# Kernel optimization log

Hardware: AMD Instinct MI355X
Metric: run time of the kernel (lower is better)

The kernel has to match this reference:

```python
import jax, jax.numpy as jnp
import numpy as np

N, C, H, W = 4, 256, 100, 100
COUT, G, EPS = 256, 32, 1e-5
K = 9  # 3x3 kernel positions

# regular 3x3 grid: row0 = dy, row1 = dx (mmcv offset convention)
REG = jnp.array([[-1,-1,-1,0,0,0,1,1,1],
                 [-1, 0, 1,-1,0,1,-1,0,1]], dtype=jnp.float32)  # (2,9)
KY = jnp.array([0,0,0,1,1,1,2,2,2], dtype=jnp.float32)
KX = jnp.array([0,1,2,0,1,2,0,1,2], dtype=jnp.float32)


def conv3x3(x, w, b):
    out = jax.lax.conv_general_dilated(x, w, window_strides=(1,1),
                                       padding=((1,1),(1,1)),
                                       dimension_numbers=('NCHW','OIHW','NCHW'))
    return out + b[None, :, None, None]


def setup_inputs() -> dict:
    key = jax.random.key(0)
    ks = jax.random.split(key, 7)
    x = jax.random.normal(ks[0], (N, C, H, W), dtype=jnp.float32)
    w_tm = jax.random.normal(ks[1], (4, C, 3, 3), dtype=jnp.float32) * 0.01
    b_tm = jnp.zeros((4,), dtype=jnp.float32)
    w_tr = jax.random.normal(ks[2], (2, C, 3, 3), dtype=jnp.float32) * 0.01
    b_tr = jnp.zeros((2,), dtype=jnp.float32)
    w_def = jax.random.normal(ks[3], (COUT, C, 3, 3), dtype=jnp.float32) * (1.0 / np.sqrt(C * 9.0))
    gn_w = 1.0 + 0.1 * jax.random.normal(ks[4], (COUT,), dtype=jnp.float32)
    gn_b = 0.1 * jax.random.normal(ks[5], (COUT,), dtype=jnp.float32)
    return dict(x=x, w_tm=w_tm, b_tm=b_tm, w_tr=w_tr, b_tr=b_tr,
                w_def=w_def, gn_w=gn_w, gn_b=gn_b)


def _compute_offsets(x, w_tm, b_tm, w_tr, b_tr):
    tm = conv3x3(x, w_tm, b_tm)                      # (N,4,H,W)
    tr = conv3x3(x, w_tr, b_tr)                      # (N,2,H,W)
    A = tm.transpose(0, 2, 3, 1).reshape(N, H, W, 2, 2)
    off = jnp.einsum('nhwij,jk->nhwik', A, REG) - REG  # (N,H,W,2,9)
    dy = (off[:, :, :, 0, :] + tr[:, 0][..., None]).transpose(0, 3, 1, 2)  # (N,9,H,W)
    dx = (off[:, :, :, 1, :] + tr[:, 1][..., None]).transpose(0, 3, 1, 2)
    return dy, dx


def _bilinear_sample(img, ys, xs):
    # img: (C,H,W); ys/xs: (9,H,W) float sampling coords; zero pad outside.
    y0 = jnp.floor(ys); x0 = jnp.floor(xs)
    wy = ys - y0; wx = xs - x0
    y0i = y0.astype(jnp.int32); x0i = x0.astype(jnp.int32)
    def gather(yi, xi):
        valid = (yi >= 0) & (yi < H) & (xi >= 0) & (xi < W)
        yc = jnp.clip(yi, 0, H - 1); xc = jnp.clip(xi, 0, W - 1)
        return img[:, yc, xc] * valid[None].astype(img.dtype)  # (C,9,H,W)
    v00 = gather(y0i,     x0i)
    v01 = gather(y0i,     x0i + 1)
    v10 = gather(y0i + 1, x0i)
    v11 = gather(y0i + 1, x0i + 1)
    return (v00 * (1 - wy) * (1 - wx) + v01 * (1 - wy) * wx
            + v10 * wy * (1 - wx) + v11 * wy * wx)


def _forward(x, w_tm, b_tm, w_tr, b_tr, w_def, gn_w, gn_b):
    dy, dx = _compute_offsets(x, w_tm, b_tm, w_tr, b_tr)
    # sampling positions: p*stride - pad + k*dil + offset  (stride=1, pad=dil=1)
    ys = jnp.arange(H, dtype=jnp.float32)[None, :, None] - 1.0 + KY[:, None, None] + dy
    xs = jnp.arange(W, dtype=jnp.float32)[None, None, :] - 1.0 + KX[:, None, None] + dx
    sampled = jax.vmap(_bilinear_sample)(x, ys, xs)       # (N,C,9,H,W)
    out = jnp.einsum('nckhw,ock->nohw', sampled, w_def.reshape(COUT, C, K))
    # GroupNorm(32) + ReLU
    g = out.reshape(N, G, (COUT // G) * H * W)
    mu = g.mean(axis=2, keepdims=True)
    var = g.var(axis=2, keepdims=True)
    g = (g - mu) * jax.lax.rsqrt(var + EPS)
    out = g.reshape(N, COUT, H, W) * gn_w[None, :, None, None] + gn_b[None, :, None, None]
    return jax.nn.relu(out)


def reference(x, w_tm, b_tm, w_tr, b_tr, w_def, gn_w, gn_b):
    return _forward(x, w_tm, b_tm, w_tr, b_tr, w_def, gn_w, gn_b)
```

## Files before the change

### kernel.cpp

```cpp
#include <hip/hip_runtime.h>
#include <math.h>

#define C_IN  256
#define HH    100
#define WW    100
#define HW    10000
#define NBAT  4
#define COUTC 256
#define K9    9
#define GG    32
#define TYN   13
#define TXN   9
#define NT2   117
#define NWG   468
#define EPSF  1e-5f

typedef _Float16 f16x8 __attribute__((ext_vector_type(8)));
typedef _Float16 h2v   __attribute__((ext_vector_type(2)));
typedef float    f32x4 __attribute__((ext_vector_type(4)));

__global__ void __launch_bounds__(256) k0_weights(const float* __restrict__ wd,
                                                  const float* __restrict__ w_tm,
                                                  const float* __restrict__ w_tr,
                                                  _Float16* __restrict__ wf,
                                                  _Float16* __restrict__ wf6) {
  const int b = blockIdx.x;
  if (b < 2304) {
    const int i = b * 256 + threadIdx.x;
    const int j  = i & 7;
    const int l  = (i >> 3) & 63;
    const int ot = (i >> 9) & 15;
    const int q  = i >> 13;
    const int tap = q >> 3, cg = q & 7;
    const int o = ot * 16 + (l & 15);
    const int c = cg * 32 + (l >> 4) * 8 + j;
    wf[i] = (_Float16)wd[((size_t)o * C_IN + c) * K9 + tap];
  } else {
    const int i = (b - 2304) * 256 + threadIdx.x;
    const int j = i & 7, l = (i >> 3) & 63, q = i >> 9;
    const int tap = q >> 3, cg = q & 7;
    const int o = l & 15;
    const int c = cg * 32 + (l >> 4) * 8 + j;
    float v = 0.f;
    if (o < 4)      v = w_tm[((size_t)o * C_IN + c) * K9 + tap];
    else if (o < 6) v = w_tr[((size_t)(o - 4) * C_IN + c) * K9 + tap];
    wf6[i] = (_Float16)v;
  }
}

__global__ void __launch_bounds__(256) kt_nhwc(const float* __restrict__ x,
                                               _Float16* __restrict__ xh) {
  __shared__ float T[64][65];
  const int b = blockIdx.x;
  const int n = b / (4 * 157);
  const int r = b % (4 * 157);
  const int cg = r / 157, tile = r % 157;
  const int pbase = tile * 64, c0 = cg * 64;
  const int tid = threadIdx.x, lane = tid & 63, wv = tid >> 6;

#pragma unroll 4
  for (int i = 0; i < 16; ++i) {
    const int c = c0 + wv * 16 + i;
    const int pix = pbase + lane;
    T[wv * 16 + i][lane] = (pix < HW) ? x[((size_t)n * C_IN + c) * HW + pix] : 0.f;
  }
  __syncthreads();

  const int cl = tid & 15;
#pragma unroll
  for (int j = 0; j < 4; ++j) {
    const int pxl = (tid >> 4) + j * 16;
    const int pix = pbase + pxl;
    if (pix < HW) {
      const float v0 = T[cl * 4 + 0][pxl], v1 = T[cl * 4 + 1][pxl];
      const float v2 = T[cl * 4 + 2][pxl], v3 = T[cl * 4 + 3][pxl];
      uint2 pk;
      h2v a = {(_Float16)v0, (_Float16)v1};
      h2v bq = {(_Float16)v2, (_Float16)v3};
      pk.x = __builtin_bit_cast(unsigned, a);
      pk.y = __builtin_bit_cast(unsigned, bq);
      *(uint2*)(xh + ((size_t)n * HW + pix) * C_IN + c0 + cl * 4) = pk;
    }
  }
}

#define RAW_BARRIER()                                                         \
  asm volatile("s_waitcnt lgkmcnt(0)" ::: "memory");                          \
  __builtin_amdgcn_sched_barrier(0);                                          \
  __builtin_amdgcn_s_barrier();                                               \
  __builtin_amdgcn_sched_barrier(0);

__global__ void __launch_bounds__(256) k1_off(
    const _Float16* __restrict__ xh, const _Float16* __restrict__ wf6,
    const float* __restrict__ b_tm, const float* __restrict__ b_tr,
    float* __restrict__ posy, float* __restrict__ posx) {
  const int ob = blockIdx.x;
  const int xcd = ob & 7, loc = ob >> 3;
  const int sblk = (xcd < 1 ? xcd * 79 : 79 + (xcd - 1) * 78) + loc;
  const int tid = threadIdx.x, lane = tid & 63, wv = tid >> 6;
  const int s = sblk * 4 + wv;
  const int n = s / 625, strip = s % 625;
  const int ps = strip * 16;
  const int px = ps + (lane & 15);
  const int h = px / WW, w = px % WW;
  const char* xbase = (const char*)(xh + (size_t)n * HW * C_IN) + (lane >> 4) * 16;

  int nbA, nbB; bool vA, vB;
#define K1NB(T_, NB, V)                                                       \
  { const int y = h + (T_) / 3 - 1, xx = w + (T_) % 3 - 1;                    \
    V = ((unsigned)y < (unsigned)HH) && ((unsigned)xx < (unsigned)WW);        \
    NB = (V ? (y * WW + xx) : 0) * 512; }

  uint4 q0, q1, q2, q3;
  K1NB(0, nbA, vA)
  nbB = nbA; vB = vA;
  q0 = *(const uint4*)(xbase + nbA + 0 * 64);
  q1 = *(const uint4*)(xbase + nbA + 1 * 64);
  q2 = *(const uint4*)(xbase + nbA + 2 * 64);
  q3 = *(const uint4*)(xbase + nbA + 3 * 64);
  f16x8 afA = *(const f16x8*)(wf6 + (size_t)0 * 512 + lane * 8);
  f16x8 afB = *(const f16x8*)(wf6 + (size_t)1 * 512 + lane * 8);

  f32x4 acc = (f32x4)(0.f);
  const uint4 z4 = {0u, 0u, 0u, 0u};

#define K1SUB(CG, Q, AF)                                                      \
  {                                                                           \
    const int p = t * 8 + (CG);                                               \
    uint4 bq = vA ? Q : z4;                                                   \
    f16x8 bf = __builtin_bit_cast(f16x8, bq);                                 \
    if ((CG) == 2) { K1NB((t < 8 ? t + 1 : 8), nbB, vB) }                     \
    if ((CG) < 4) { Q = *(const uint4*)(xbase + nbA + ((CG) + 4) * 64); }     \
    else if (t < 8) { Q = *(const uint4*)(xbase + nbB + ((CG) - 4) * 64); }   \
    acc = __builtin_amdgcn_mfma_f32_16x16x32_f16(AF, bf, acc, 0, 0, 0);       \
    if ((CG) < 6 || t < 8)                                                    \
      AF = *(const f16x8*)(wf6 + (size_t)(p + 2) * 512 + lane * 8);           \
  }

  for (int t = 0; t < 9; ++t) {
    K1SUB(0, q0, afA) K1SUB(1, q1, afB) K1SUB(2, q2, afA) K1SUB(3, q3, afB)
    K1SUB(4, q0, afA) K1SUB(5, q1, afB) K1SUB(6, q2, afA) K1SUB(7, q3, afB)
    nbA = nbB; vA = vB;
  }

  const float t0v = __shfl(acc[0], (lane & 15) + 16);
  const float t1v = __shfl(acc[1], (lane & 15) + 16);
  if (lane < 16) {
    const float A00 = acc[0] + b_tm[0], A01 = acc[1] + b_tm[1];
    const float A10 = acc[2] + b_tm[2], A11 = acc[3] + b_tm[3];
    const float t0 = t0v + b_tr[0], t1 = t1v + b_tr[1];
    const float fh = (float)h, fw = (float)w;
#pragma unroll
    for (int k = 0; k < 9; ++k) {
      const float ry = (float)(k / 3 - 1);
      const float rx = (float)(k % 3 - 1);
      posy[((size_t)n * K9 + k) * HW + px] = fh + t0 + A00 * ry + A01 * rx;
      posx[((size_t)n * K9 + k) * HW + px] = fw + t1 + A10 * ry + A11 * rx;
    }
  }
}

__global__ void __launch_bounds__(512, 4) k2_deform(
    const _Float16* __restrict__ xh, const _Float16* __restrict__ wfrag,
    const float* __restrict__ posy, const float* __restrict__ posx,
    float* __restrict__ out, float* __restrict__ part) {
  __shared__ __align__(16) char Bs[2 * 96 * 64];
  __shared__ __align__(16) unsigned int ctab[864 * 8];

  const int ob = blockIdx.x;
  const int xcd = ob & 7, loc = ob >> 3;
  const int wg = (xcd < 4 ? xcd * 59 : 236 + (xcd - 4) * 58) + loc;
  const int n = wg / NT2, rem = wg % NT2;
  const int ty = rem / TXN, tx = rem % TXN;

  const int tid = threadIdx.x, lane = tid & 63, wv = tid >> 6;
  const bool stg = tid < 384;
  const int px_s = tid >> 2, qo = tid & 3;
  const int wsw = (((qo + (px_s >> 1)) & 3) << 4);
  const int rpx = lane & 15, rko = lane >> 4;
  const int rsw = (((rko + (rpx >> 1)) & 3) << 4);

  for (int s = tid; s < 864; s += 512) {
    const int tap = s / 96, j = s % 96;
    const int row = ty * 8 + j / 12, col = tx * 12 + j % 12;
    const bool pvv = (row < HH) && (col < WW);
    const int mpa = pvv ? (row * WW + col) : 0;
    float ys = posy[((size_t)n * K9 + tap) * HW + mpa];
    float xs = posx[((size_t)n * K9 + tap) * HW + mpa];
    if (!pvv) { ys = -1e4f; xs = -1e4f; }
    const float y0f = floorf(ys), x0f = floorf(xs);
    const float wy = ys - y0f, wx = xs - x0f;
    const int iy0 = (int)y0f, ix0 = (int)x0f;
    const bool vy0 = ((unsigned)iy0 < (unsigned)HH);
    const bool vy1 = ((unsigned)(iy0 + 1) < (unsigned)HH);
    const bool vx0 = ((unsigned)ix0 < (unsigned)WW);
    const bool vx1 = ((unsigned)(ix0 + 1) < (unsigned)WW);
    const bool v0 = vy0 && vx0, v1 = vy0 && vx1;
    const bool v2 = vy1 && vx0, v3 = vy1 && vx1;
    uint4 oa, wa;
    oa.x = (v0 ? (iy0 * WW + ix0) : 0) * 512u;
    oa.y = (v1 ? (iy0 * WW + ix0 + 1) : 0) * 512u;
    oa.z = (v2 ? ((iy0 + 1) * WW + ix0) : 0) * 512u;
    oa.w = (v3 ? ((iy0 + 1) * WW + ix0 + 1) : 0) * 512u;
    const float g0 = v0 ? (1.f - wy) * (1.f - wx) : 0.f;
    const float g1 = v1 ? (1.f - wy) * wx : 0.f;
    const float g2 = v2 ? wy * (1.f - wx) : 0.f;
    const float g3 = v3 ? wy * wx : 0.f;
    const _Float16 h0 = (_Float16)g0, h1 = (_Float16)g1;
    const _Float16 h2_ = (_Float16)g2, h3 = (_Float16)g3;
    wa.x = __builtin_bit_cast(unsigned, (h2v){h0, h0});
    wa.y = __builtin_bit_cast(unsigned, (h2v){h1, h1});
    wa.z = __builtin_bit_cast(unsigned, (h2v){h2_, h2_});
    wa.w = __builtin_bit_cast(unsigned, (h2v){h3, h3});
    uint4* cp = (uint4*)&ctab[s * 8];
    cp[0] = oa;
    cp[1] = wa;
  }
  __syncthreads();

  const char* xbase = (const char*)(xh + (size_t)n * HW * C_IN);

  uint4 O, Wt, c0, c1, c2, c3;
  f16x8 aA0, aA1, aB0, aB1;

#define ISSUE(S)                                                              \
  if (stg) {                                                                  \
    const uint4* ce = (const uint4*)&ctab[(((S) >> 3) * 96 + px_s) * 8];      \
    O = ce[0];                                                                \
    Wt = ce[1];                                                               \
    const int choff = ((S) & 7) * 64 + qo * 16;                               \
    c0 = *(const uint4*)(xbase + O.x + choff);                                \
    c1 = *(const uint4*)(xbase + O.y + choff);                                \
    c2 = *(const uint4*)(xbase + O.z + choff);                                \
    c3 = *(const uint4*)(xbase + O.w + choff);                                \
  }

#define CW1(c)                                                                \
  __builtin_bit_cast(unsigned,                                                \
      (h2v)(w0 * __builtin_bit_cast(h2v, c0.c) +                              \
            w1 * __builtin_bit_cast(h2v, c1.c) +                              \
            w2 * __builtin_bit_cast(h2v, c2.c) +                              \
            w3 * __builtin_bit_cast(h2v, c3.c)))

#define COMBINE_WRITE(BUFW)                                                   \
  if (stg) {                                                                  \
    h2v w0 = __builtin_bit_cast(h2v, Wt.x), w1 = __builtin_bit_cast(h2v, Wt.y); \
    h2v w2 = __builtin_bit_cast(h2v, Wt.z), w3 = __builtin_bit_cast(h2v, Wt.w); \
    uint4 sv;                                                                 \
    sv.x = CW1(x);                                                            \
    sv.y = CW1(y);                                                            \
    sv.z = CW1(z);                                                            \
    sv.w = CW1(w);                                                            \
    *(uint4*)(Bs + (BUFW) * 6144 + px_s * 64 + wsw) = sv;                     \
  }

#define LOADA(A0_, A1_, CK)                                                   \
  {                                                                           \
    const _Float16* wfp = wfrag + (((size_t)(CK) * 16 + wv * 2) * 64 + lane) * 8; \
    A0_ = *(const f16x8*)(wfp);                                               \
    A1_ = *(const f16x8*)(wfp + 512);                                         \
  }

  f32x4 acc[2][6];
#pragma unroll
  for (int ot = 0; ot < 2; ++ot)
#pragma unroll
    for (int bt = 0; bt < 6; ++bt) acc[ot][bt] = (f32x4)(0.f);

#define MF(a, bx, o_, b_) \
  acc[o_][b_] = __builtin_amdgcn_mfma_f32_16x16x32_f16(a, bx, acc[o_][b_], 0, 0, 0);

#define MFMA12(A0_, A1_, BUF)                                                 \
  {                                                                           \
    const char* bb = Bs + (BUF) * 6144 + rpx * 64 + rsw;                      \
    f16x8 b0 = *(const f16x8*)(bb);                                           \
    f16x8 b1 = *(const f16x8*)(bb + 1024);                                    \
    f16x8 b2 = *(const f16x8*)(bb + 2048);                                    \
    f16x8 b3 = *(const f16x8*)(bb + 3072);                                    \
    f16x8 b4 = *(const f16x8*)(bb + 4096);                                    \
    f16x8 b5 = *(const f16x8*)(bb + 5120);                                    \
    __builtin_amdgcn_s_setprio(1);                                            \
    MF(A0_, b0, 0, 0) MF(A1_, b0, 1, 0)                                       \
    MF(A0_, b1, 0, 1) MF(A1_, b1, 1, 1)                                       \
    MF(A0_, b2, 0, 2) MF(A1_, b2, 1, 2)                                       \
    MF(A0_, b3, 0, 3) MF(A1_, b3, 1, 3)                                       \
    MF(A0_, b4, 0, 4) MF(A1_, b4, 1, 4)                                       \
    MF(A0_, b5, 0, 5) MF(A1_, b5, 1, 5)                                       \
    __builtin_amdgcn_s_setprio(0);                                            \
  }

  ISSUE(0)
  COMBINE_WRITE(0)
  ISSUE(1)
  LOADA(aA0, aA1, 0)
  LOADA(aB0, aB1, 1)
  RAW_BARRIER()

  for (int sp = 0; sp < 35; ++sp) {
    const int s0 = 2 * sp, s1 = 2 * sp + 1;
    MFMA12(aA0, aA1, 0)
    LOADA(aA0, aA1, s0 + 2)
    COMBINE_WRITE(1)
    ISSUE(s0 + 2)
    RAW_BARRIER()
    MFMA12(aB0, aB1, 1)
    LOADA(aB0, aB1, s1 + 2)
    COMBINE_WRITE(0)
    ISSUE(s1 + 2)
    RAW_BARRIER()
  }
  MFMA12(aA0, aA1, 0)
  COMBINE_WRITE(1)
  RAW_BARRIER()
  MFMA12(aB0, aB1, 1)

  float* grA = (float*)ctab;
  float* grB = grA + 1024;
  const int colb = lane & 15, prow = (lane >> 4) * 4;
#pragma unroll
  for (int ot = 0; ot < 2; ++ot) {
    float s1 = 0.f, s2 = 0.f;
#pragma unroll
    for (int bt = 0; bt < 6; ++bt) {
      const int jj = bt * 16 + colb;
      const int row = ty * 8 + jj / 12, col = tx * 12 + jj % 12;
      const f32x4 a = acc[ot][bt];
      if (row < HH && col < WW) {
        float* op = out + ((size_t)(n * COUTC + wv * 32 + ot * 16 + prow)) * HW +
                    row * WW + col;
        op[0] = a[0];
        op[HW] = a[1];
        op[2 * HW] = a[2];
        op[3 * HW] = a[3];
      }
      s1 += a[0] + a[1] + a[2] + a[3];
      s2 += a[0] * a[0] + a[1] * a[1] + a[2] * a[2] + a[3] * a[3];
    }
    grA[(wv * 2 + ot) * 64 + lane] = s1;
    grB[(wv * 2 + ot) * 64 + lane] = s2;
  }
  __syncthreads();
  if (tid < 32) {
    const int wv2 = tid >> 2, ot2 = (tid >> 1) & 1, hb = tid & 1;
    float a1 = 0.f, a2 = 0.f;
#pragma unroll 8
    for (int l = 0; l < 32; ++l) {
      a1 += grA[(wv2 * 2 + ot2) * 64 + hb * 32 + l];
      a2 += grB[(wv2 * 2 + ot2) * 64 + hb * 32 + l];
    }
    float* pp = part + (((size_t)n * NT2 + rem) * GG + tid) * 2;
    pp[0] = a1;
    pp[1] = a2;
  }
}

__global__ void __launch_bounds__(64) k3_stats(const float* __restrict__ part,
                                               float* __restrict__ stats) {
  const int b = blockIdx.x;
  const int n = b >> 5, g = b & 31;
  double s = 0.0, q = 0.0;
  for (int i = threadIdx.x; i < NT2; i += 64) {
    const float* pp = part + (((size_t)n * NT2 + i) * GG + g) * 2;
    s += pp[0];
    q += pp[1];
  }
#pragma unroll
  for (int off = 32; off > 0; off >>= 1) {
    s += __shfl_down(s, off);
    q += __shfl_down(q, off);
  }
  if (threadIdx.x == 0) {
    const double cnt = 8.0 * (double)HW;
    const double mean = s / cnt;
    const double var = q / cnt - mean * mean;
    stats[b * 2 + 0] = (float)mean;
    stats[b * 2 + 1] = (float)(1.0 / sqrt(var + (double)EPSF));
  }
}

__global__ void __launch_bounds__(256) k4_norm(float* __restrict__ out,
                                               const float* __restrict__ stats,
                                               const float* __restrict__ gw,
                                               const float* __restrict__ gb) {
  const size_t i4 = (size_t)blockIdx.x * 256 + threadIdx.x;
  const size_t idx = i4 * 4;
  const int n = (int)(idx / ((size_t)COUTC * HW));
  const int r = (int)(idx % ((size_t)COUTC * HW));
  const int o = r / HW;
  const int g = o >> 3;
  const float mean = stats[(n * GG + g) * 2 + 0];
  const float rs = stats[(n * GG + g) * 2 + 1];
  const float sc = rs * gw[o];
  const float sh = gb[o] - mean * sc;
  float4 v = *(float4*)(out + idx);
  v.x = fmaxf(fmaf(v.x, sc, sh), 0.f);
  v.y = fmaxf(fmaf(v.y, sc, sh), 0.f);
  v.z = fmaxf(fmaf(v.z, sc, sh), 0.f);
  v.w = fmaxf(fmaf(v.w, sc, sh), 0.f);
  *(float4*)(out + idx) = v;
}

extern "C" void kernel_launch(void* const* d_in, const int* in_sizes, int n_in,
                              void* d_out, int out_size, void* d_ws, size_t ws_size,
                              hipStream_t stream) {
  const float* x    = (const float*)d_in[0];
  const float* w_tm = (const float*)d_in[1];
  const float* b_tm = (const float*)d_in[2];
  const float* w_tr = (const float*)d_in[3];
  const float* b_tr = (const float*)d_in[4];
  const float* w_def = (const float*)d_in[5];
  const float* gn_w = (const float*)d_in[6];
  const float* gn_b = (const float*)d_in[7];
  float* out = (float*)d_out;
  float* ws = (float*)d_ws;

  float* posy  = ws;
  float* posx  = ws + 360000;
  _Float16* wfrag = (_Float16*)(ws + 720000);
  _Float16* wf6   = (_Float16*)(ws + 1014912);
  _Float16* xh    = (_Float16*)(ws + 1033344);
  float* part  = ws + 6153344;
  float* stats = ws + 6183296;

  hipLaunchKernelGGL(k0_weights, dim3(2448), dim3(256), 0, stream,
                     w_def, w_tm, w_tr, wfrag, wf6);
  hipLaunchKernelGGL(kt_nhwc, dim3(2512), dim3(256), 0, stream, x, xh);
  hipLaunchKernelGGL(k1_off, dim3(625), dim3(256), 0, stream,
                     xh, wf6, b_tm, b_tr, posy, posx);
  hipLaunchKernelGGL(k2_deform, dim3(NWG), dim3(512), 0, stream,
                     xh, wfrag, posy, posx, out, part);
  hipLaunchKernelGGL(k3_stats, dim3(NBAT * GG), dim3(64), 0, stream, part, stats);
  hipLaunchKernelGGL(k4_norm, dim3(10000), dim3(256), 0, stream,
                     out, stats, gn_w, gn_b);
}
```

Baseline: 137.4 us.

## Merge prep kernels, fold stats into norm, deepen gather prefetch, nontemporal stores

Combines the weight repack and the NHWC transpose into one launch, and removes the separate GroupNorm stats kernel by having every norm block reduce the per-tile partials itself. In the deform kernel, the gather pipeline now runs one stage further ahead using two register sets, and the combine weights are read from LDS only when needed. Conv outputs are written with nontemporal stores. The aim is fewer launches and better hiding of gather latency, at the cost of redundant partial reductions in every norm block (float instead of double), more live registers, and a nontemporal hint on data that k4 reads back.

New measurement: 204.2 us. 1.49x slower.

```diff
diff --git a/kernel.cpp b/kernel.cpp
--- a/kernel.cpp
+++ b/kernel.cpp
@@ -19,39 +19,40 @@
 typedef _Float16 h2v   __attribute__((ext_vector_type(2)));
 typedef float    f32x4 __attribute__((ext_vector_type(4)));
 
-__global__ void __launch_bounds__(256) k0_weights(const float* __restrict__ wd,
-                                                  const float* __restrict__ w_tm,
-                                                  const float* __restrict__ w_tr,
-                                                  _Float16* __restrict__ wf,
-                                                  _Float16* __restrict__ wf6) {
+__global__ void __launch_bounds__(256) kt_prep(const float* __restrict__ x,
+                                               const float* __restrict__ wd,
+                                               const float* __restrict__ w_tm,
+                                               const float* __restrict__ w_tr,
+                                               _Float16* __restrict__ xh,
+                                               _Float16* __restrict__ wf,
+                                               _Float16* __restrict__ wf6) {
   const int b = blockIdx.x;
-  if (b < 2304) {
-    const int i = b * 256 + threadIdx.x;
-    const int j  = i & 7;
-    const int l  = (i >> 3) & 63;
-    const int ot = (i >> 9) & 15;
-    const int q  = i >> 13;
-    const int tap = q >> 3, cg = q & 7;
-    const int o = ot * 16 + (l & 15);
-    const int c = cg * 32 + (l >> 4) * 8 + j;
-    wf[i] = (_Float16)wd[((size_t)o * C_IN + c) * K9 + tap];
-  } else {
-    const int i = (b - 2304) * 256 + threadIdx.x;
-    const int j = i & 7, l = (i >> 3) & 63, q = i >> 9;
-    const int tap = q >> 3, cg = q & 7;
-    const int o = l & 15;
-    const int c = cg * 32 + (l >> 4) * 8 + j;
-    float v = 0.f;
-    if (o < 4)      v = w_tm[((size_t)o * C_IN + c) * K9 + tap];
-    else if (o < 6) v = w_tr[((size_t)(o - 4) * C_IN + c) * K9 + tap];
-    wf6[i] = (_Float16)v;
-  }
-}
-
-__global__ void __launch_bounds__(256) kt_nhwc(const float* __restrict__ x,
-                                               _Float16* __restrict__ xh) {
+  if (b >= 2512) {
+    const int bb = b - 2512;
+    if (bb < 2304) {
+      const int i = bb * 256 + threadIdx.x;
+      const int j  = i & 7;
+      const int l  = (i >> 3) & 63;
+      const int ot = (i >> 9) & 15;
+      const int q  = i >> 13;
+      const int tap = q >> 3, cg = q & 7;
+      const int o = ot * 16 + (l & 15);
+      const int c = cg * 32 + (l >> 4) * 8 + j;
+      wf[i] = (_Float16)wd[((size_t)o * C_IN + c) * K9 + tap];
+    } else {
+      const int i = (bb - 2304) * 256 + threadIdx.x;
+      const int j = i & 7, l = (i >> 3) & 63, q = i >> 9;
+      const int tap = q >> 3, cg = q & 7;
+      const int o = l & 15;
+      const int c = cg * 32 + (l >> 4) * 8 + j;
+      float v = 0.f;
+      if (o < 4)      v = w_tm[((size_t)o * C_IN + c) * K9 + tap];
+      else if (o < 6) v = w_tr[((size_t)(o - 4) * C_IN + c) * K9 + tap];
+      wf6[i] = (_Float16)v;
+    }
+    return;
+  }
   __shared__ float T[64][65];
-  const int b = blockIdx.x;
   const int n = b / (4 * 157);
   const int r = b % (4 * 157);
   const int cg = r / 157, tile = r % 157;
@@ -220,38 +221,39 @@
 
   const char* xbase = (const char*)(xh + (size_t)n * HW * C_IN);
 
-  uint4 O, Wt, c0, c1, c2, c3;
+  uint4 cA0, cA1, cA2, cA3, cB0, cB1, cB2, cB3;
   f16x8 aA0, aA1, aB0, aB1;
 
-#define ISSUE(S)                                                              \
+#define ISSUE(S, C0, C1, C2, C3)                                              \
   if (stg) {                                                                  \
-    const uint4* ce = (const uint4*)&ctab[(((S) >> 3) * 96 + px_s) * 8];      \
-    O = ce[0];                                                                \
-    Wt = ce[1];                                                               \
+    const uint4 Ox = *(const uint4*)&ctab[(((S) >> 3) * 96 + px_s) * 8];      \
     const int choff = ((S) & 7) * 64 + qo * 16;                               \
-    c0 = *(const uint4*)(xbase + O.x + choff);                                \
-    c1 = *(const uint4*)(xbase + O.y + choff);                                \
-    c2 = *(const uint4*)(xbase + O.z + choff);                                \
-    c3 = *(const uint4*)(xbase + O.w + choff);                                \
-  }
-
-#define CW1(c)                                                                \
+    C0 = *(const uint4*)(xbase + Ox.x + choff);                               \
+    C1 = *(const uint4*)(xbase + Ox.y + choff);                               \
+    C2 = *(const uint4*)(xbase + Ox.z + choff);                               \
+    C3 = *(const uint4*)(xbase + Ox.w + choff);                               \
+  }
+
+#define CW1(c, C0, C1, C2, C3)                                                \
   __builtin_bit_cast(unsigned,                                                \
-      (h2v)(w0 * __builtin_bit_cast(h2v, c0.c) +                              \
-            w1 * __builtin_bit_cast(h2v, c1.c) +                              \
-            w2 * __builtin_bit_cast(h2v, c2.c) +                              \
-            w3 * __builtin_bit_cast(h2v, c3.c)))
-
-#define COMBINE_WRITE(BUFW)                                                   \
+      (h2v)(w0 * __builtin_bit_cast(h2v, C0.c) +                              \
+            w1 * __builtin_bit_cast(h2v, C1.c) +                              \
+            w2 * __builtin_bit_cast(h2v, C2.c) +                              \
+            w3 * __builtin_bit_cast(h2v, C3.c)))
+
+#define COMBINE_WRITE(S, C0, C1, C2, C3)                                      \
   if (stg) {                                                                  \
-    h2v w0 = __builtin_bit_cast(h2v, Wt.x), w1 = __builtin_bit_cast(h2v, Wt.y); \
-    h2v w2 = __builtin_bit_cast(h2v, Wt.z), w3 = __builtin_bit_cast(h2v, Wt.w); \
+    const uint4 Wt = *(const uint4*)&ctab[(((S) >> 3) * 96 + px_s) * 8 + 4];  \
+    const h2v w0 = __builtin_bit_cast(h2v, Wt.x);                             \
+    const h2v w1 = __builtin_bit_cast(h2v, Wt.y);                             \
+    const h2v w2 = __builtin_bit_cast(h2v, Wt.z);                             \
+    const h2v w3 = __builtin_bit_cast(h2v, Wt.w);                             \
     uint4 sv;                                                                 \
-    sv.x = CW1(x);                                                            \
-    sv.y = CW1(y);                                                            \
-    sv.z = CW1(z);                                                            \
-    sv.w = CW1(w);                                                            \
-    *(uint4*)(Bs + (BUFW) * 6144 + px_s * 64 + wsw) = sv;                     \
+    sv.x = CW1(x, C0, C1, C2, C3);                                            \
+    sv.y = CW1(y, C0, C1, C2, C3);                                            \
+    sv.z = CW1(z, C0, C1, C2, C3);                                            \
+    sv.w = CW1(w, C0, C1, C2, C3);                                            \
+    *(uint4*)(Bs + ((S) & 1) * 6144 + px_s * 64 + wsw) = sv;                  \
   }
 
 #define LOADA(A0_, A1_, CK)                                                   \
@@ -289,9 +291,10 @@
     __builtin_amdgcn_s_setprio(0);                                            \
   }
 
-  ISSUE(0)
-  COMBINE_WRITE(0)
-  ISSUE(1)
+  ISSUE(0, cA0, cA1, cA2, cA3)
+  COMBINE_WRITE(0, cA0, cA1, cA2, cA3)
+  ISSUE(1, cA0, cA1, cA2, cA3)
+  ISSUE(2, cB0, cB1, cB2, cB3)
   LOADA(aA0, aA1, 0)
   LOADA(aB0, aB1, 1)
   RAW_BARRIER()
@@ -300,17 +303,17 @@
     const int s0 = 2 * sp, s1 = 2 * sp + 1;
     MFMA12(aA0, aA1, 0)
     LOADA(aA0, aA1, s0 + 2)
-    COMBINE_WRITE(1)
-    ISSUE(s0 + 2)
+    COMBINE_WRITE(s0 + 1, cA0, cA1, cA2, cA3)
+    ISSUE(s0 + 3, cA0, cA1, cA2, cA3)
     RAW_BARRIER()
     MFMA12(aB0, aB1, 1)
     LOADA(aB0, aB1, s1 + 2)
-    COMBINE_WRITE(0)
-    ISSUE(s1 + 2)
+    COMBINE_WRITE(s1 + 1, cB0, cB1, cB2, cB3)
+    if (sp < 34) { ISSUE(s1 + 3, cB0, cB1, cB2, cB3) }
     RAW_BARRIER()
   }
   MFMA12(aA0, aA1, 0)
-  COMBINE_WRITE(1)
+  COMBINE_WRITE(71, cA0, cA1, cA2, cA3)
   RAW_BARRIER()
   MFMA12(aB0, aB1, 1)
 
@@ -328,10 +331,10 @@
       if (row < HH && col < WW) {
         float* op = out + ((size_t)(n * COUTC + wv * 32 + ot * 16 + prow)) * HW +
                     row * WW + col;
-        op[0] = a[0];
-        op[HW] = a[1];
-        op[2 * HW] = a[2];
-        op[3 * HW] = a[3];
+        __builtin_nontemporal_store(a[0], op);
+        __builtin_nontemporal_store(a[1], op + HW);
+        __builtin_nontemporal_store(a[2], op + 2 * HW);
+        __builtin_nontemporal_store(a[3], op + 3 * HW);
       }
       s1 += a[0] + a[1] + a[2] + a[3];
       s2 += a[0] * a[0] + a[1] * a[1] + a[2] * a[2] + a[3] * a[3];
@@ -354,42 +357,55 @@
   }
 }
 
-__global__ void __launch_bounds__(64) k3_stats(const float* __restrict__ part,
-                                               float* __restrict__ stats) {
-  const int b = blockIdx.x;
-  const int n = b >> 5, g = b & 31;
-  double s = 0.0, q = 0.0;
-  for (int i = threadIdx.x; i < NT2; i += 64) {
-    const float* pp = part + (((size_t)n * NT2 + i) * GG + g) * 2;
-    s += pp[0];
-    q += pp[1];
-  }
-#pragma unroll
-  for (int off = 32; off > 0; off >>= 1) {
-    s += __shfl_down(s, off);
-    q += __shfl_down(q, off);
-  }
-  if (threadIdx.x == 0) {
-    const double cnt = 8.0 * (double)HW;
-    const double mean = s / cnt;
-    const double var = q / cnt - mean * mean;
-    stats[b * 2 + 0] = (float)mean;
-    stats[b * 2 + 1] = (float)(1.0 / sqrt(var + (double)EPSF));
-  }
-}
-
 __global__ void __launch_bounds__(256) k4_norm(float* __restrict__ out,
-                                               const float* __restrict__ stats,
+                                               const float* __restrict__ part,
                                                const float* __restrict__ gw,
                                                const float* __restrict__ gb) {
-  const size_t i4 = (size_t)blockIdx.x * 256 + threadIdx.x;
-  const size_t idx = i4 * 4;
-  const int n = (int)(idx / ((size_t)COUTC * HW));
-  const int r = (int)(idx % ((size_t)COUTC * HW));
-  const int o = r / HW;
+  const int b = blockIdx.x;
+  const int tid = threadIdx.x;
+  const size_t idx0 = (size_t)b * 1024;
+  const int n = (int)(idx0 / ((size_t)COUTC * HW));
+  const int r0 = (int)(idx0 % ((size_t)COUTC * HW));
+  const int gfirst = (r0 / HW) >> 3;
+  const int glast = ((r0 + 1023) / HW) >> 3;
+  const int ngrp = (glast > gfirst) ? 2 : 1;
+
+  __shared__ float rr[4][2];
+  __shared__ float sm[2][2];
+
+  for (int wgrp = 0; wgrp < ngrp; ++wgrp) {
+    const int g = wgrp ? glast : gfirst;
+    float s1 = 0.f, s2 = 0.f;
+    if (tid < NT2) {
+      const float* pp = part + (((size_t)n * NT2 + tid) * GG + g) * 2;
+      s1 = pp[0];
+      s2 = pp[1];
+    }
+#pragma unroll
+    for (int off = 32; off > 0; off >>= 1) {
+      s1 += __shfl_down(s1, off);
+      s2 += __shfl_down(s2, off);
+    }
+    if ((tid & 63) == 0) { rr[tid >> 6][0] = s1; rr[tid >> 6][1] = s2; }
+    __syncthreads();
+    if (tid == 0) {
+      const float a1 = rr[0][0] + rr[1][0] + rr[2][0] + rr[3][0];
+      const float a2 = rr[0][1] + rr[1][1] + rr[2][1] + rr[3][1];
+      const float cnt = 8.0f * (float)HW;
+      const float mean = a1 / cnt;
+      const float var = a2 / cnt - mean * mean;
+      sm[wgrp][0] = mean;
+      sm[wgrp][1] = rsqrtf(var + EPSF);
+    }
+    __syncthreads();
+  }
+
+  const size_t idx = idx0 + (size_t)tid * 4;
+  const int o = (int)((idx % ((size_t)COUTC * HW)) / HW);
   const int g = o >> 3;
-  const float mean = stats[(n * GG + g) * 2 + 0];
-  const float rs = stats[(n * GG + g) * 2 + 1];
+  const int which = (g == gfirst) ? 0 : 1;
+  const float mean = sm[which][0];
+  const float rs = sm[which][1];
   const float sc = rs * gw[o];
   const float sh = gb[o] - mean * sc;
   float4 v = *(float4*)(out + idx);
@@ -420,16 +436,13 @@
   _Float16* wf6   = (_Float16*)(ws + 1014912);
   _Float16* xh    = (_Float16*)(ws + 1033344);
   float* part  = ws + 6153344;
-  float* stats = ws + 6183296;
-
-  hipLaunchKernelGGL(k0_weights, dim3(2448), dim3(256), 0, stream,
-                     w_def, w_tm, w_tr, wfrag, wf6);
-  hipLaunchKernelGGL(kt_nhwc, dim3(2512), dim3(256), 0, stream, x, xh);
+
+  hipLaunchKernelGGL(kt_prep, dim3(4960), dim3(256), 0, stream,
+                     x, w_def, w_tm, w_tr, xh, wfrag, wf6);
   hipLaunchKernelGGL(k1_off, dim3(625), dim3(256), 0, stream,
                      xh, wf6, b_tm, b_tr, posy, posx);
   hipLaunchKernelGGL(k2_deform, dim3(NWG), dim3(512), 0, stream,
                      xh, wfrag, posy, posx, out, part);
-  hipLaunchKernelGGL(k3_stats, dim3(NBAT * GG), dim3(64), 0, stream, part, stats);
   hipLaunchKernelGGL(k4_norm, dim3(10000), dim3(256), 0, stream,
-                     out, stats, gn_w, gn_b);
+                     out, part, gn_w, gn_b);
 }
```
